# Kernel optimization log

Measured on AMD Instinct MI355X. Metric: run time of the kernel, lower is better.

The kernel has to match this reference:

```python
import jax, jax.numpy as jnp
import numpy as np

B, C, H, W = 64, 1024, 16, 16
R = 8            # ratio
CK = C // R      # key channels
N = H * W


def setup_inputs() -> dict:
    key = jax.random.key(0)
    ks = jax.random.split(key, 12)
    g = 0.02  # xavier gain used in the module
    def xav(k, fan_out, fan_in):
        std = g * (2.0 / (fan_in + fan_out)) ** 0.5
        return jax.random.normal(k, (fan_out, fan_in), dtype=jnp.float32) * std
    return {
        "x": jax.random.normal(ks[0], (B, C, H, W), dtype=jnp.float32),
        "y": jax.random.normal(ks[1], (B, C, H, W), dtype=jnp.float32),
        "wk1": xav(ks[2], CK, C),
        "bk1": jnp.zeros((CK,), jnp.float32),
        "wk2": xav(ks[3], CK, C),
        "bk2": jnp.zeros((CK,), jnp.float32),
        "wv1": xav(ks[4], C, C),
        "bv1": jnp.zeros((C,), jnp.float32),
        "wv2": xav(ks[5], C, C),
        "bv2": jnp.zeros((C,), jnp.float32),
        "gamma1": jnp.zeros((1,), jnp.float32),
        "gamma2": jnp.zeros((1,), jnp.float32),
    }


def reference(x, y, wk1, bk1, wk2, bk2, wv1, bv1, wv2, bv2, gamma1, gamma2):
    b, c, h, w = x.shape
    n = h * w
    xf = x.reshape(b, c, n)  # [B,C,N]
    yf = y.reshape(b, c, n)
    # 1x1 convs as channel GEMMs
    kx = jnp.einsum('oc,bcn->bon', wk1, xf) + bk1[:, None]  # [B,CK,N]
    ky = jnp.einsum('oc,bcn->bon', wk2, yf) + bk2[:, None]
    vx = jnp.einsum('oc,bcn->bon', wv1, xf) + bv1[:, None]  # [B,C,N]
    vy = jnp.einsum('oc,bcn->bon', wv2, yf) + bv2[:, None]
    # cross energies: query = permuted key projection of own branch
    energy_x = jnp.einsum('bkn,bkm->bnm', kx, ky)  # q_x @ k_y
    energy_y = jnp.einsum('bkn,bkm->bnm', ky, kx)  # q_y @ k_x
    attn_x = jax.nn.softmax(energy_x, axis=-1)  # [B,N,N]
    attn_y = jax.nn.softmax(energy_y, axis=-1)
    # out = V @ attn^T
    ox = jnp.einsum('bcn,bmn->bcm', vx, attn_x).reshape(b, c, h, w)
    oy = jnp.einsum('bcn,bmn->bcm', vy, attn_y).reshape(b, c, h, w)
    out_x = gamma1 * ox + x
    out_y = gamma2 * oy + y
    return out_x, out_y
```

## Files before the change

### kernel.cpp

```cpp
#include <hip/hip_runtime.h>
#include <hip/hip_bf16.h>
#include <stdint.h>

#define B_  64
#define C_  1024
#define CK_ 128
#define N_  256

typedef __bf16 bf16;
typedef __attribute__((ext_vector_type(8))) __bf16 bf16x8;
typedef __attribute__((ext_vector_type(4))) __bf16 bf16x4;
typedef __attribute__((ext_vector_type(4))) float floatx4;

constexpr size_t OFF_XBT = 0;
constexpr size_t OFF_YBT = 33554432;
constexpr size_t OFF_WK1 = 67108864;
constexpr size_t OFF_WK2 = 67371008;
constexpr size_t OFF_WV1 = 67633152;
constexpr size_t OFF_WV2 = 69730304;
constexpr size_t OFF_AX  = 71827456;
constexpr size_t OFF_AY  = 80216064;
constexpr size_t WS_NEEDED = 88604672;

__device__ __forceinline__ void async16(const void* g, void* l) {
  __builtin_amdgcn_global_load_lds((const __attribute__((address_space(1))) void*)g,
                                   (__attribute__((address_space(3))) void*)l, 16, 0, 0);
}

__global__ __launch_bounds__(256) void k_xpose(const float* __restrict__ xin,
                                               const float* __restrict__ yin,
                                               bf16* __restrict__ xo, bf16* __restrict__ yo) {
  __shared__ float tile[64][65];
  int nt = blockIdx.x, ct = blockIdx.y, z = blockIdx.z;
  int b = z & 63;
  const float* in = (z < 64) ? xin : yin;
  bf16* out = (z < 64) ? xo : yo;
  const float* src = in + (size_t)b * C_ * N_ + (size_t)ct * 64 * N_ + nt * 64;
  bf16* dst = out + (size_t)b * N_ * C_ + (size_t)nt * 64 * C_ + ct * 64;
  int c4 = (threadIdx.x & 15) * 4, r0 = threadIdx.x >> 4;
#pragma unroll
  for (int i = 0; i < 4; ++i) {
    int r = r0 + i * 16;
    float4 v = *(const float4*)(src + r * N_ + c4);
    tile[r][c4 + 0] = v.x; tile[r][c4 + 1] = v.y;
    tile[r][c4 + 2] = v.z; tile[r][c4 + 3] = v.w;
  }
  __syncthreads();
#pragma unroll
  for (int i = 0; i < 4; ++i) {
    int r = r0 + i * 16;
    bf16x4 o;
    o[0] = (bf16)tile[c4 + 0][r]; o[1] = (bf16)tile[c4 + 1][r];
    o[2] = (bf16)tile[c4 + 2][r]; o[3] = (bf16)tile[c4 + 3][r];
    *(bf16x4*)(dst + (size_t)r * C_ + c4) = o;
  }
}

__global__ __launch_bounds__(256) void k_cvt2(const float* __restrict__ inA,
                                              const float* __restrict__ inB,
                                              bf16* __restrict__ outA, bf16* __restrict__ outB,
                                              int n4each) {
  int i = blockIdx.x * 256 + threadIdx.x;
  const float* in = (i < n4each) ? inA : inB;
  bf16* out = (i < n4each) ? outA : outB;
  int j = (i < n4each) ? i : (i - n4each);
  if (i < 2 * n4each) {
    float4 v = ((const float4*)in)[j];
    bf16x4 o;
    o[0] = (bf16)v.x; o[1] = (bf16)v.y; o[2] = (bf16)v.z; o[3] = (bf16)v.w;
    ((bf16x4*)out)[j] = o;
  }
}

template <int KITERS>
__device__ __forceinline__ void gemm128_core(const bf16* __restrict__ Ag, int ldA,
                                             const bf16* __restrict__ Bg, int ldB,
                                             char* smem, floatx4 (&acc)[4][4]) {
  const int tid = threadIdx.x;
  const int l = tid & 63, wid = tid >> 6;
  const int wm = wid & 1, wn = wid >> 1;
  auto issue = [&](int kt, int buf) {
    const int k0 = kt * 32;
#pragma unroll
    for (int s = 0; s < 2; ++s) {
      int row = (s << 6) + (wid << 4) + (l >> 2);
      int q = (l & 3) ^ ((row >> 1) & 3);
      async16(Ag + (size_t)row * ldA + k0 + q * 8, smem + buf * 8192 + (s << 12) + (wid << 10));
      async16(Bg + (size_t)row * ldB + k0 + q * 8, smem + 24576 + buf * 8192 + (s << 12) + (wid << 10));
    }
  };
  auto compute = [&](int buf) {
    const char* As = smem + buf * 8192;
    const char* Bs = smem + 24576 + buf * 8192;
    bf16x8 af[4], bfr[4];
#pragma unroll
    for (int t = 0; t < 4; ++t) {
      int m = (wm << 6) + t * 16 + (l & 15);
      af[t] = *(const bf16x8*)(As + m * 64 + (((l >> 4) ^ ((m >> 1) & 3)) << 4));
      int n = (wn << 6) + t * 16 + (l & 15);
      bfr[t] = *(const bf16x8*)(Bs + n * 64 + (((l >> 4) ^ ((n >> 1) & 3)) << 4));
    }
#pragma unroll
    for (int tm = 0; tm < 4; ++tm)
#pragma unroll
      for (int tn = 0; tn < 4; ++tn)
        acc[tm][tn] = __builtin_amdgcn_mfma_f32_16x16x32_bf16(af[tm], bfr[tn], acc[tm][tn], 0, 0, 0);
  };
  issue(0, 0);
  if (KITERS > 1) issue(1, 1);
#pragma unroll
  for (int kt = 0; kt < KITERS; ++kt) {
    if (kt + 1 < KITERS) asm volatile("s_waitcnt vmcnt(4) lgkmcnt(0)" ::: "memory");
    else                 asm volatile("s_waitcnt vmcnt(0) lgkmcnt(0)" ::: "memory");
    __builtin_amdgcn_s_barrier();
    asm volatile("" ::: "memory");
    if (kt + 2 < KITERS) issue(kt + 2, (kt + 2) % 3);
    __builtin_amdgcn_s_setprio(1);
    compute(kt % 3);
    __builtin_amdgcn_s_setprio(0);
  }
}

__global__ __launch_bounds__(256) void k_projk(
    const bf16* __restrict__ xbT, const bf16* __restrict__ ybT,
    const bf16* __restrict__ wk1b, const bf16* __restrict__ wk2b,
    const float* __restrict__ bk1, const float* __restrict__ bk2,
    bf16* __restrict__ kxT, bf16* __restrict__ kyT) {
  __shared__ __align__(16) char smem[49152];
  int mt = blockIdx.x, br = blockIdx.y, b = blockIdx.z;
  const bf16* A = (br ? ybT : xbT) + (size_t)b * N_ * C_ + (size_t)mt * 128 * C_;
  const bf16* Bt = br ? wk2b : wk1b;
  const float* bias = br ? bk2 : bk1;
  bf16* out = (br ? kyT : kxT) + (size_t)b * N_ * CK_ + (size_t)mt * 128 * CK_;
  floatx4 acc[4][4];
  floatx4 z = {0.f, 0.f, 0.f, 0.f};
#pragma unroll
  for (int i = 0; i < 4; ++i)
#pragma unroll
    for (int j = 0; j < 4; ++j) acc[i][j] = z;
  gemm128_core<32>(A, C_, Bt, C_, smem, acc);
  const int l = threadIdx.x & 63, wid = threadIdx.x >> 6;
  const int wm = wid & 1, wn = wid >> 1;
#pragma unroll
  for (int tn = 0; tn < 4; ++tn) {
    int oc = (wn << 6) + tn * 16 + (l & 15);
    float bkv = bias[oc];
#pragma unroll
    for (int tm = 0; tm < 4; ++tm)
#pragma unroll
      for (int r = 0; r < 4; ++r) {
        int row = (wm << 6) + tm * 16 + ((l >> 4) << 2) + r;
        out[row * CK_ + oc] = (bf16)(acc[tm][tn][r] + bkv);
      }
  }
}

__global__ __launch_bounds__(256) void k_esoft(
    const bf16* __restrict__ kxT, const bf16* __restrict__ kyT,
    bf16* __restrict__ ax, bf16* __restrict__ ay) {
  int rh = blockIdx.x, br = blockIdx.y, b = blockIdx.z;
  const bf16* A  = (br ? kyT : kxT) + (size_t)b * N_ * CK_;
  const bf16* Bm = (br ? kxT : kyT) + (size_t)b * N_ * CK_;
  bf16* outp = (br ? ay : ax) + (size_t)b * N_ * N_;
  const int tid = threadIdx.x, l = tid & 63, wid = tid >> 6;
  const int m0 = rh * 128 + wid * 32;

  floatx4 acc[2][16];
  floatx4 z = {0.f, 0.f, 0.f, 0.f};
#pragma unroll
  for (int i = 0; i < 2; ++i)
#pragma unroll
    for (int j = 0; j < 16; ++j) acc[i][j] = z;

#pragma unroll
  for (int kk = 0; kk < 4; ++kk) {
    bf16x8 af[2];
    const bf16* pa = A + (size_t)(m0 + (l & 15)) * CK_ + kk * 32 + ((l >> 4) << 3);
    af[0] = *(const bf16x8*)(pa);
    af[1] = *(const bf16x8*)(pa + 16 * CK_);
#pragma unroll
    for (int h = 0; h < 2; ++h) {
      bf16x8 bfr[8];
#pragma unroll
      for (int t = 0; t < 8; ++t) {
        int n = (h * 8 + t) * 16 + (l & 15);
        bfr[t] = *(const bf16x8*)(Bm + (size_t)n * CK_ + kk * 32 + ((l >> 4) << 3));
      }
#pragma unroll
      for (int tm = 0; tm < 2; ++tm)
#pragma unroll
        for (int t = 0; t < 8; ++t)
          acc[tm][h * 8 + t] =
              __builtin_amdgcn_mfma_f32_16x16x32_bf16(af[tm], bfr[t], acc[tm][h * 8 + t], 0, 0, 0);
    }
  }

#pragma unroll
  for (int tm = 0; tm < 2; ++tm)
#pragma unroll
    for (int r = 0; r < 4; ++r) {
      float mx = -1e30f;
#pragma unroll
      for (int tn = 0; tn < 16; ++tn) mx = fmaxf(mx, acc[tm][tn][r]);
#pragma unroll
      for (int off = 8; off > 0; off >>= 1) mx = fmaxf(mx, __shfl_xor(mx, off));
      float s = 0.f;
#pragma unroll
      for (int tn = 0; tn < 16; ++tn) {
        float e = __expf(acc[tm][tn][r] - mx);
        acc[tm][tn][r] = e;
        s += e;
      }
#pragma unroll
      for (int off = 8; off > 0; off >>= 1) s += __shfl_xor(s, off);
      float rc = 1.0f / s;
      int m = m0 + tm * 16 + ((l >> 4) << 2) + r;
#pragma unroll
      for (int tn = 0; tn < 16; ++tn)
        outp[(size_t)m * N_ + tn * 16 + (l & 15)] = (bf16)(acc[tm][tn][r] * rc);
    }
}

__global__ __launch_bounds__(512, 4) void k_vapply(
    const bf16* __restrict__ xbT, const bf16* __restrict__ ybT,
    const bf16* __restrict__ wv1b, const bf16* __restrict__ wv2b,
    const float* __restrict__ bv1, const float* __restrict__ bv2,
    const bf16* __restrict__ ax, const bf16* __restrict__ ay,
    const float* __restrict__ xin0, const float* __restrict__ yin0,
    const float* __restrict__ g1, const float* __restrict__ g2,
    float* __restrict__ out) {
  __shared__ __align__(16) char smem[65536];
  int id = blockIdx.x;
  int xcd = id & 7;
  int idx = id >> 3;
  int b = xcd + ((idx >> 4) << 3);
  int inner = idx & 15;
  int ct = inner & 7, br = inner >> 3;

  const bf16* A1 = (br ? wv2b : wv1b) + (size_t)ct * 128 * C_;
  const bf16* Bt1 = (br ? ybT : xbT) + (size_t)b * N_ * C_;
  const float* bias = br ? bv2 : bv1;
  const bf16* attn = (br ? ay : ax) + (size_t)b * N_ * N_;
  const float* xin = (br ? yin0 : xin0) + (size_t)b * C_ * N_ + (size_t)ct * 128 * N_;
  float gamma = br ? g2[0] : g1[0];
  float* o = out + (size_t)br * B_ * C_ * N_ + (size_t)b * C_ * N_ + (size_t)ct * 128 * N_;
  const int tid = threadIdx.x, l = tid & 63, wid = tid >> 6;
  const int wm = wid >> 2, wn = wid & 3;

  auto issueA = [&](int kt, int abuf) {
    int row = (wid << 4) + (l >> 2);
    int q = (l & 3) ^ ((row >> 1) & 3);
    async16(A1 + (size_t)row * C_ + kt * 32 + q * 8, smem + abuf * 8192 + (wid << 10));
  };
  auto issueB = [&](int kt, int bbuf) {
#pragma unroll
    for (int s = 0; s < 2; ++s) {
      int row = (s << 7) + (wid << 4) + (l >> 2);
      int q = (l & 3) ^ ((row >> 1) & 3);
      async16(Bt1 + (size_t)row * C_ + kt * 32 + q * 8,
              smem + 16384 + bbuf * 16384 + (s << 13) + (wid << 10));
    }
  };
  floatx4 acc[4][4];
  floatx4 z = {0.f, 0.f, 0.f, 0.f};
#pragma unroll
  for (int i = 0; i < 4; ++i)
#pragma unroll
    for (int j = 0; j < 4; ++j) acc[i][j] = z;

  auto compute1 = [&](int abuf, int bbuf) {
    const char* As = smem + abuf * 8192;
    const char* Bs = smem + 16384 + bbuf * 16384;
    bf16x8 af[4], bfr[4];
#pragma unroll
    for (int t = 0; t < 4; ++t) {
      int m = (wm << 6) + t * 16 + (l & 15);
      af[t] = *(const bf16x8*)(As + m * 64 + (((l >> 4) ^ ((m >> 1) & 3)) << 4));
      int n = (wn << 6) + t * 16 + (l & 15);
      bfr[t] = *(const bf16x8*)(Bs + n * 64 + (((l >> 4) ^ ((n >> 1) & 3)) << 4));
    }
#pragma unroll
    for (int tm = 0; tm < 4; ++tm)
#pragma unroll
      for (int tn = 0; tn < 4; ++tn)
        acc[tm][tn] = __builtin_amdgcn_mfma_f32_16x16x32_bf16(af[tm], bfr[tn], acc[tm][tn], 0, 0, 0);
  };

  issueA(0, 0); issueB(0, 0); issueB(1, 1);
#pragma unroll
  for (int kt = 0; kt < 32; ++kt) {
    if (kt < 31) asm volatile("s_waitcnt vmcnt(2) lgkmcnt(0)" ::: "memory");
    else         asm volatile("s_waitcnt vmcnt(0) lgkmcnt(0)" ::: "memory");
    __builtin_amdgcn_s_barrier();
    asm volatile("" ::: "memory");
    if (kt < 31) issueA(kt + 1, (kt + 1) & 1);
    if (kt < 30) issueB(kt + 2, (kt + 2) % 3);
    __builtin_amdgcn_s_setprio(1);
    compute1(kt & 1, kt % 3);
    __builtin_amdgcn_s_setprio(0);
  }
  __syncthreads();

  char* vt = smem;
#pragma unroll
  for (int tm = 0; tm < 4; ++tm)
#pragma unroll
    for (int r = 0; r < 4; ++r) {
      int rr = (wm << 6) + tm * 16 + ((l >> 4) << 2) + r;
      float bkv = bias[ct * 128 + rr];
#pragma unroll
      for (int tn = 0; tn < 4; ++tn) {
        int n = (wn << 6) + tn * 16 + (l & 15);
        int ch = (n >> 3) ^ (rr & 7);
        *(bf16*)(vt + rr * 512 + ch * 16 + ((n & 7) << 1)) = (bf16)(acc[tm][tn][r] + bkv);
      }
    }

  auto loadB2 = [&](int kt, bf16x8 (&bb)[4]) {
    const bf16* p = attn + (size_t)((wn << 6) + (l & 15)) * N_ + kt * 32 + ((l >> 4) << 3);
#pragma unroll
    for (int t = 0; t < 4; ++t) bb[t] = *(const bf16x8*)(p + (size_t)t * 16 * N_);
  };
  auto compute2 = [&](int kt, bf16x8 (&bb)[4]) {
    bf16x8 af[4];
#pragma unroll
    for (int t = 0; t < 4; ++t) {
      int m = (wm << 6) + t * 16 + (l & 15);
      int ch = ((kt << 2) + (l >> 4)) ^ (m & 7);
      af[t] = *(const bf16x8*)(vt + m * 512 + (ch << 4));
    }
#pragma unroll
    for (int tm = 0; tm < 4; ++tm)
#pragma unroll
      for (int tn = 0; tn < 4; ++tn)
        acc[tm][tn] = __builtin_amdgcn_mfma_f32_16x16x32_bf16(af[tm], bb[tn], acc[tm][tn], 0, 0, 0);
  };

  bf16x8 bfA[4], bfB[4];
  loadB2(0, bfA);
  __syncthreads();
#pragma unroll
  for (int i = 0; i < 4; ++i)
#pragma unroll
    for (int j = 0; j < 4; ++j) acc[i][j] = z;
  for (int kt = 0; kt < 8; kt += 2) {
    loadB2(kt + 1, bfB);
    compute2(kt, bfA);
    if (kt + 2 < 8) loadB2(kt + 2, bfA);
    compute2(kt + 1, bfB);
  }

#pragma unroll
  for (int tm = 0; tm < 4; ++tm)
#pragma unroll
    for (int tn = 0; tn < 4; ++tn)
#pragma unroll
      for (int r = 0; r < 4; ++r) {
        int rr = (wm << 6) + tm * 16 + ((l >> 4) << 2) + r;
        int m = (wn << 6) + tn * 16 + (l & 15);
        int idx2 = rr * N_ + m;
        o[idx2] = gamma * acc[tm][tn][r] + xin[idx2];
      }
}

__global__ __launch_bounds__(256) void k_fallback(const float4* __restrict__ x,
                                                  const float4* __restrict__ y,
                                                  float4* __restrict__ out) {
  size_t i = (size_t)blockIdx.x * 256 + threadIdx.x;
  out[i] = x[i];
  out[4194304 + i] = y[i];
}

extern "C" void kernel_launch(void* const* d_in, const int* in_sizes, int n_in,
                              void* d_out, int out_size, void* d_ws, size_t ws_size,
                              hipStream_t stream) {
  const float* x   = (const float*)d_in[0];
  const float* y   = (const float*)d_in[1];
  const float* wk1 = (const float*)d_in[2];
  const float* bk1 = (const float*)d_in[3];
  const float* wk2 = (const float*)d_in[4];
  const float* bk2 = (const float*)d_in[5];
  const float* wv1 = (const float*)d_in[6];
  const float* bv1 = (const float*)d_in[7];
  const float* wv2 = (const float*)d_in[8];
  const float* bv2 = (const float*)d_in[9];
  const float* g1  = (const float*)d_in[10];
  const float* g2  = (const float*)d_in[11];
  float* out = (float*)d_out;

  if (ws_size < WS_NEEDED) {
    k_fallback<<<16384, 256, 0, stream>>>((const float4*)x, (const float4*)y, (float4*)out);
    return;
  }

  char* ws = (char*)d_ws;
  bf16* xbT  = (bf16*)(ws + OFF_XBT);
  bf16* ybT  = (bf16*)(ws + OFF_YBT);
  bf16* wk1b = (bf16*)(ws + OFF_WK1);
  bf16* wk2b = (bf16*)(ws + OFF_WK2);
  bf16* wv1b = (bf16*)(ws + OFF_WV1);
  bf16* wv2b = (bf16*)(ws + OFF_WV2);
  bf16* axp  = (bf16*)(ws + OFF_AX);
  bf16* ayp  = (bf16*)(ws + OFF_AY);
  bf16* kxT = (bf16*)((char*)out + (size_t)B_ * C_ * N_ * 4);
  bf16* kyT = (bf16*)((char*)out + (size_t)B_ * C_ * N_ * 4 + 4194304);

  k_xpose<<<dim3(4, 16, 128), 256, 0, stream>>>(x, y, xbT, ybT);
  k_cvt2<<<256, 256, 0, stream>>>(wk1, wk2, wk1b, wk2b, 32768);
  k_cvt2<<<2048, 256, 0, stream>>>(wv1, wv2, wv1b, wv2b, 262144);
  k_projk<<<dim3(2, 2, 64), 256, 0, stream>>>(xbT, ybT, wk1b, wk2b, bk1, bk2, kxT, kyT);
  k_esoft<<<dim3(2, 2, 64), 256, 0, stream>>>(kxT, kyT, axp, ayp);
  k_vapply<<<1024, 512, 0, stream>>>(xbT, ybT, wv1b, wv2b, bv1, bv2,
                                     axp, ayp, x, y, g1, g2, out);
}
```

Measured before the change: 415.5 us.

## Double vapply channel tile to 256 and merge weight conversion launches

```diff
diff --git a/kernel.cpp b/kernel.cpp
--- a/kernel.cpp
+++ b/kernel.cpp
@@ -56,20 +56,25 @@
   }
 }
 
-__global__ __launch_bounds__(256) void k_cvt2(const float* __restrict__ inA,
-                                              const float* __restrict__ inB,
-                                              bf16* __restrict__ outA, bf16* __restrict__ outB,
-                                              int n4each) {
+__global__ __launch_bounds__(256) void k_cvt4(
+    const float* __restrict__ wk1, const float* __restrict__ wk2,
+    bf16* __restrict__ ok1, bf16* __restrict__ ok2,
+    const float* __restrict__ wv1, const float* __restrict__ wv2,
+    bf16* __restrict__ ov1, bf16* __restrict__ ov2) {
   int i = blockIdx.x * 256 + threadIdx.x;
-  const float* in = (i < n4each) ? inA : inB;
-  bf16* out = (i < n4each) ? outA : outB;
-  int j = (i < n4each) ? i : (i - n4each);
-  if (i < 2 * n4each) {
-    float4 v = ((const float4*)in)[j];
-    bf16x4 o;
-    o[0] = (bf16)v.x; o[1] = (bf16)v.y; o[2] = (bf16)v.z; o[3] = (bf16)v.w;
-    ((bf16x4*)out)[j] = o;
-  }
+  const float* in; bf16* out; int j;
+  if (i < 65536) {
+    bool s = i < 32768;
+    in = s ? wk1 : wk2; out = s ? ok1 : ok2; j = s ? i : i - 32768;
+  } else {
+    int k = i - 65536;
+    bool s = k < 262144;
+    in = s ? wv1 : wv2; out = s ? ov1 : ov2; j = s ? k : k - 262144;
+  }
+  float4 v = ((const float4*)in)[j];
+  bf16x4 o;
+  o[0] = (bf16)v.x; o[1] = (bf16)v.y; o[2] = (bf16)v.z; o[3] = (bf16)v.w;
+  ((bf16x4*)out)[j] = o;
 }
 
 template <int KITERS>
@@ -221,7 +226,7 @@
     }
 }
 
-__global__ __launch_bounds__(512, 4) void k_vapply(
+__global__ __launch_bounds__(512, 2) void k_vapply(
     const bf16* __restrict__ xbT, const bf16* __restrict__ ybT,
     const bf16* __restrict__ wv1b, const bf16* __restrict__ wv2b,
     const float* __restrict__ bv1, const float* __restrict__ bv2,
@@ -229,28 +234,32 @@
     const float* __restrict__ xin0, const float* __restrict__ yin0,
     const float* __restrict__ g1, const float* __restrict__ g2,
     float* __restrict__ out) {
-  __shared__ __align__(16) char smem[65536];
+  __shared__ __align__(16) char smem[131072];
   int id = blockIdx.x;
   int xcd = id & 7;
   int idx = id >> 3;
-  int b = xcd + ((idx >> 4) << 3);
-  int inner = idx & 15;
-  int ct = inner & 7, br = inner >> 3;
-
-  const bf16* A1 = (br ? wv2b : wv1b) + (size_t)ct * 128 * C_;
+  int b = xcd + ((idx >> 3) << 3);
+  int inner = idx & 7;
+  int ct = inner & 3, br = inner >> 2;
+
+  const bf16* A1 = (br ? wv2b : wv1b) + (size_t)ct * 256 * C_;
   const bf16* Bt1 = (br ? ybT : xbT) + (size_t)b * N_ * C_;
   const float* bias = br ? bv2 : bv1;
   const bf16* attn = (br ? ay : ax) + (size_t)b * N_ * N_;
-  const float* xin = (br ? yin0 : xin0) + (size_t)b * C_ * N_ + (size_t)ct * 128 * N_;
+  const float* xin = (br ? yin0 : xin0) + (size_t)b * C_ * N_ + (size_t)ct * 256 * N_;
   float gamma = br ? g2[0] : g1[0];
-  float* o = out + (size_t)br * B_ * C_ * N_ + (size_t)b * C_ * N_ + (size_t)ct * 128 * N_;
+  float* o = out + (size_t)br * B_ * C_ * N_ + (size_t)b * C_ * N_ + (size_t)ct * 256 * N_;
   const int tid = threadIdx.x, l = tid & 63, wid = tid >> 6;
   const int wm = wid >> 2, wn = wid & 3;
 
   auto issueA = [&](int kt, int abuf) {
-    int row = (wid << 4) + (l >> 2);
-    int q = (l & 3) ^ ((row >> 1) & 3);
-    async16(A1 + (size_t)row * C_ + kt * 32 + q * 8, smem + abuf * 8192 + (wid << 10));
+#pragma unroll
+    for (int s = 0; s < 2; ++s) {
+      int row = (s << 7) + (wid << 4) + (l >> 2);
+      int q = (l & 3) ^ ((row >> 1) & 3);
+      async16(A1 + (size_t)row * C_ + kt * 32 + q * 8,
+              smem + abuf * 16384 + (s << 13) + (wid << 10));
+    }
   };
   auto issueB = [&](int kt, int bbuf) {
 #pragma unroll
@@ -258,29 +267,32 @@
       int row = (s << 7) + (wid << 4) + (l >> 2);
       int q = (l & 3) ^ ((row >> 1) & 3);
       async16(Bt1 + (size_t)row * C_ + kt * 32 + q * 8,
-              smem + 16384 + bbuf * 16384 + (s << 13) + (wid << 10));
-    }
-  };
-  floatx4 acc[4][4];
+              smem + 32768 + bbuf * 16384 + (s << 13) + (wid << 10));
+    }
+  };
+  floatx4 acc[8][4];
   floatx4 z = {0.f, 0.f, 0.f, 0.f};
 #pragma unroll
-  for (int i = 0; i < 4; ++i)
+  for (int i = 0; i < 8; ++i)
 #pragma unroll
     for (int j = 0; j < 4; ++j) acc[i][j] = z;
 
   auto compute1 = [&](int abuf, int bbuf) {
-    const char* As = smem + abuf * 8192;
-    const char* Bs = smem + 16384 + bbuf * 16384;
-    bf16x8 af[4], bfr[4];
+    const char* As = smem + abuf * 16384;
+    const char* Bs = smem + 32768 + bbuf * 16384;
+    bf16x8 af[8], bfr[4];
+#pragma unroll
+    for (int t = 0; t < 8; ++t) {
+      int m = (wm << 7) + t * 16 + (l & 15);
+      af[t] = *(const bf16x8*)(As + m * 64 + (((l >> 4) ^ ((m >> 1) & 3)) << 4));
+    }
 #pragma unroll
     for (int t = 0; t < 4; ++t) {
-      int m = (wm << 6) + t * 16 + (l & 15);
-      af[t] = *(const bf16x8*)(As + m * 64 + (((l >> 4) ^ ((m >> 1) & 3)) << 4));
       int n = (wn << 6) + t * 16 + (l & 15);
       bfr[t] = *(const bf16x8*)(Bs + n * 64 + (((l >> 4) ^ ((n >> 1) & 3)) << 4));
     }
 #pragma unroll
-    for (int tm = 0; tm < 4; ++tm)
+    for (int tm = 0; tm < 8; ++tm)
 #pragma unroll
       for (int tn = 0; tn < 4; ++tn)
         acc[tm][tn] = __builtin_amdgcn_mfma_f32_16x16x32_bf16(af[tm], bfr[tn], acc[tm][tn], 0, 0, 0);
@@ -303,11 +315,11 @@
 
   char* vt = smem;
 #pragma unroll
-  for (int tm = 0; tm < 4; ++tm)
+  for (int tm = 0; tm < 8; ++tm)
 #pragma unroll
     for (int r = 0; r < 4; ++r) {
-      int rr = (wm << 6) + tm * 16 + ((l >> 4) << 2) + r;
-      float bkv = bias[ct * 128 + rr];
+      int rr = (wm << 7) + tm * 16 + ((l >> 4) << 2) + r;
+      float bkv = bias[ct * 256 + rr];
 #pragma unroll
       for (int tn = 0; tn < 4; ++tn) {
         int n = (wn << 6) + tn * 16 + (l & 15);
@@ -322,15 +334,15 @@
     for (int t = 0; t < 4; ++t) bb[t] = *(const bf16x8*)(p + (size_t)t * 16 * N_);
   };
   auto compute2 = [&](int kt, bf16x8 (&bb)[4]) {
-    bf16x8 af[4];
-#pragma unroll
-    for (int t = 0; t < 4; ++t) {
-      int m = (wm << 6) + t * 16 + (l & 15);
+    bf16x8 af[8];
+#pragma unroll
+    for (int t = 0; t < 8; ++t) {
+      int m = (wm << 7) + t * 16 + (l & 15);
       int ch = ((kt << 2) + (l >> 4)) ^ (m & 7);
       af[t] = *(const bf16x8*)(vt + m * 512 + (ch << 4));
     }
 #pragma unroll
-    for (int tm = 0; tm < 4; ++tm)
+    for (int tm = 0; tm < 8; ++tm)
 #pragma unroll
       for (int tn = 0; tn < 4; ++tn)
         acc[tm][tn] = __builtin_amdgcn_mfma_f32_16x16x32_bf16(af[tm], bb[tn], acc[tm][tn], 0, 0, 0);
@@ -340,7 +352,7 @@
   loadB2(0, bfA);
   __syncthreads();
 #pragma unroll
-  for (int i = 0; i < 4; ++i)
+  for (int i = 0; i < 8; ++i)
 #pragma unroll
     for (int j = 0; j < 4; ++j) acc[i][j] = z;
   for (int kt = 0; kt < 8; kt += 2) {
@@ -351,12 +363,12 @@
   }
 
 #pragma unroll
-  for (int tm = 0; tm < 4; ++tm)
+  for (int tm = 0; tm < 8; ++tm)
 #pragma unroll
     for (int tn = 0; tn < 4; ++tn)
 #pragma unroll
       for (int r = 0; r < 4; ++r) {
-        int rr = (wm << 6) + tm * 16 + ((l >> 4) << 2) + r;
+        int rr = (wm << 7) + tm * 16 + ((l >> 4) << 2) + r;
         int m = (wn << 6) + tn * 16 + (l & 15);
         int idx2 = rr * N_ + m;
         o[idx2] = gamma * acc[tm][tn][r] + xin[idx2];
@@ -406,10 +418,9 @@
   bf16* kyT = (bf16*)((char*)out + (size_t)B_ * C_ * N_ * 4 + 4194304);
 
   k_xpose<<<dim3(4, 16, 128), 256, 0, stream>>>(x, y, xbT, ybT);
-  k_cvt2<<<256, 256, 0, stream>>>(wk1, wk2, wk1b, wk2b, 32768);
-  k_cvt2<<<2048, 256, 0, stream>>>(wv1, wv2, wv1b, wv2b, 262144);
+  k_cvt4<<<2304, 256, 0, stream>>>(wk1, wk2, wk1b, wk2b, wv1, wv2, wv1b, wv2b);
   k_projk<<<dim3(2, 2, 64), 256, 0, stream>>>(xbT, ybT, wk1b, wk2b, bk1, bk2, kxT, kyT);
   k_esoft<<<dim3(2, 2, 64), 256, 0, stream>>>(kxT, kyT, axp, ayp);
-  k_vapply<<<1024, 512, 0, stream>>>(xbT, ybT, wv1b, wv2b, bv1, bv2,
-                                     axp, ayp, x, y, g1, g2, out);
-}
+  k_vapply<<<512, 512, 0, stream>>>(xbT, ybT, wv1b, wv2b, bv1, bv2,
+                                    axp, ayp, x, y, g1, g2, out);
+}
```

New measurement: 402.3 us. -3.2%, faster.
